# Optimization experiments

Measured on AMD Instinct MI355X. Metric: run time of the kernel, lower is better.

## Reference

```python
import jax, jax.numpy as jnp
import numpy as np

B, IN, J, K = 1024, 512, 64, 8
CLAMP_MAX = 10.0

def setup_inputs() -> dict:
    key = jax.random.key(0)
    k1, k2 = jax.random.split(key)
    x = jax.random.normal(k1, (B, IN), dtype=jnp.float32)
    T = jax.random.normal(k2, (IN, J, K), dtype=jnp.float32)
    return {"x": x, "T": T}

def reference(x, T):
    # M: [B, J, K]
    M = jnp.einsum('bi,ijk->bjk', x, T)
    # pairwise diff over batch: [B, B, J, K] (matches torch broadcast M1-M2)
    diff = M[None, :, :, :] - M[:, None, :, :]
    sq = jnp.sum(diff * diff, axis=3)          # [B, B, J]
    # safe sqrt (grad 0 at 0, matching torch.norm subgradient on diagonal)
    sq_safe = jnp.where(sq > 0, sq, 1.0)
    norm = jnp.where(sq > 0, jnp.sqrt(sq_safe), 0.0)
    c = jnp.exp(-jnp.minimum(norm, CLAMP_MAX))  # clamp(max=10) then exp(-.)
    feats = jnp.sum(c, axis=1)                  # [B, J]
    return jnp.concatenate([x, feats], axis=1)  # [B, IN + J]
```

## Files before the change

kernel.cpp:

```cpp
#include <hip/hip_runtime.h>

constexpr int NB  = 1024;
constexpr int NIN = 512;
constexpr int NJ  = 64;
constexpr int NK  = 8;
constexpr int NC  = NJ * NK;
constexpr int OUTC = NIN + NJ;
constexpr float EXPN10 = 4.5399929762484854e-05f;
constexpr float FEAT_BASE = 1024.0f * EXPN10;

typedef __bf16 bf16x8 __attribute__((ext_vector_type(8)));
typedef float floatx16 __attribute__((ext_vector_type(16)));

__device__ __forceinline__ unsigned f2bf(float f) {
  unsigned u = __float_as_uint(f);
  u += 0x7FFFu + ((u >> 16) & 1u);
  return u >> 16;
}

__global__ __launch_bounds__(256) void gemm_fused(const float* __restrict__ x,
                                                  const float* __restrict__ T,
                                                  float* __restrict__ Mp,
                                                  uint4* __restrict__ Mb,
                                                  float* __restrict__ na,
                                                  float* __restrict__ out) {
  __shared__ __align__(16) ushort smem_u[2 * 64 * 136];
  ushort* Xs = smem_u;
  ushort* Ts = smem_u + 64 * 136;
  float*  Cs = (float*)smem_u;

  const int tid = threadIdx.x;
  const int b0 = blockIdx.x * 64;
  const int c0 = blockIdx.y * 64;

  const int lane = tid & 63;
  const int w    = tid >> 6;
  const int l31  = lane & 31;
  const int half = lane >> 5;
  const int arow = (w & 1) * 32 + l31;
  const int bcol = (w >> 1) * 32 + l31;

  const int pr   = tid >> 4;
  const int coff = (tid & 15) * 4;

  const int bidf = blockIdx.y * 16 + blockIdx.x;
#pragma unroll
  for (int it = 0; it < 5; ++it) {
    const int li = it * 256 + tid;
    if (li < 1152) {
      const int gi = bidf * 1152 + li;
      const int b = gi / (OUTC / 4);
      const int r = gi - b * (OUTC / 4);
      float4 v;
      if (r < NIN / 4) v = ((const float4*)x)[b * (NIN / 4) + r];
      else v = float4{FEAT_BASE, FEAT_BASE, FEAT_BASE, FEAT_BASE};
      ((float4*)out)[gi] = v;
    }
  }

  floatx16 acc = {};

  for (int z = 0; z < 4; ++z) {
    float4 av[8];
#pragma unroll
    for (int t = 0; t < 4; ++t) {
      const int u = t * 256 + tid;
      const int row = u >> 4, seg = u & 15;
      const size_t base = (size_t)(b0 + row) * NIN + z * 128 + seg * 8;
      av[2 * t]     = *(const float4*)&x[base];
      av[2 * t + 1] = *(const float4*)&x[base + 4];
    }
    float4 bv[8];
#pragma unroll
    for (int it = 0; it < 4; ++it) {
      const int k0 = it * 32 + pr * 2;
      const size_t base = (size_t)(z * 128 + k0) * NC + c0 + coff;
      bv[2 * it]     = *(const float4*)&T[base];
      bv[2 * it + 1] = *(const float4*)&T[base + NC];
    }

#pragma unroll
    for (int t = 0; t < 4; ++t) {
      const int u = t * 256 + tid;
      const int row = u >> 4, seg = u & 15;
      uint4 p;
      p.x = f2bf(av[2 * t].x) | (f2bf(av[2 * t].y) << 16);
      p.y = f2bf(av[2 * t].z) | (f2bf(av[2 * t].w) << 16);
      p.z = f2bf(av[2 * t + 1].x) | (f2bf(av[2 * t + 1].y) << 16);
      p.w = f2bf(av[2 * t + 1].z) | (f2bf(av[2 * t + 1].w) << 16);
      *(uint4*)&Xs[row * 136 + seg * 8] = p;
    }
    unsigned* Tw = (unsigned*)Ts;
#pragma unroll
    for (int it = 0; it < 4; ++it) {
      const float* lo = &bv[2 * it].x;
      const float* hi = &bv[2 * it + 1].x;
#pragma unroll
      for (int q = 0; q < 4; ++q) {
        const unsigned val = f2bf(lo[q]) | (f2bf(hi[q]) << 16);
        Tw[(coff + q) * 68 + it * 16 + pr] = val;
      }
    }

    __syncthreads();

#pragma unroll
    for (int s = 0; s < 8; ++s) {
      const bf16x8 af = *(const bf16x8*)&Xs[arow * 136 + s * 16 + half * 8];
      const bf16x8 bf = *(const bf16x8*)&Ts[bcol * 136 + s * 16 + half * 8];
      acc = __builtin_amdgcn_mfma_f32_32x32x16_bf16(af, bf, acc, 0, 0, 0);
    }
    __syncthreads();
  }

#pragma unroll
  for (int reg = 0; reg < 16; ++reg) {
    const int row = (reg & 3) + 8 * (reg >> 2) + 4 * half;
    Cs[((w & 1) * 32 + row) * 68 + (w >> 1) * 32 + l31] = acc[reg];
  }
  __syncthreads();

#pragma unroll
  for (int pass = 0; pass < 2; ++pass) {
    const int jl = (tid >> 6) + pass * 4;
    const int b  = tid & 63;
    const float4 m0 = *(const float4*)&Cs[b * 68 + jl * 8];
    const float4 m1 = *(const float4*)&Cs[b * 68 + jl * 8 + 4];
    const int j_g = blockIdx.y * 8 + jl;
    const int idx = j_g * NB + b0 + b;
    ((float4*)Mp)[idx * 2]     = m0;
    ((float4*)Mp)[idx * 2 + 1] = m1;
    float s = m0.x * m0.x;
    s = fmaf(m0.y, m0.y, s); s = fmaf(m0.z, m0.z, s); s = fmaf(m0.w, m0.w, s);
    s = fmaf(m1.x, m1.x, s); s = fmaf(m1.y, m1.y, s); s = fmaf(m1.z, m1.z, s);
    s = fmaf(m1.w, m1.w, s);
    na[idx] = s;
    uint4 pk;
    pk.x = f2bf(m0.x) | (f2bf(m0.y) << 16);
    pk.y = f2bf(m0.z) | (f2bf(m0.w) << 16);
    pk.z = f2bf(m1.x) | (f2bf(m1.y) << 16);
    pk.w = f2bf(m1.z) | (f2bf(m1.w) << 16);
    Mb[idx] = pk;
  }
}

__global__ __launch_bounds__(256) void pairwise_kernel(const uint4* __restrict__ Mb,
                                                       const float* __restrict__ na,
                                                       const float* __restrict__ Mp,
                                                       float* __restrict__ out) {
  const int j    = blockIdx.x;
  const int ag   = blockIdx.y;
  const int bh   = blockIdx.z;
  const int tid  = threadIdx.x;
  const int lane = tid & 63;
  const int w    = tid >> 6;
  const int col  = lane & 31;
  const int h    = lane >> 5;
  const int jb   = j * NB;

  __shared__ uint4 Mb_s[513];
  __shared__ float nb_s[512];
  __shared__ float na_s[128];

  const int bbeg = bh * 512;
  Mb_s[tid]       = Mb[jb + bbeg + tid];
  Mb_s[tid + 256] = Mb[jb + bbeg + tid + 256];
  nb_s[tid]       = na[jb + bbeg + tid];
  nb_s[tid + 256] = na[jb + bbeg + tid + 256];
  if (tid == 0) Mb_s[512] = uint4{0u, 0u, 0u, 0u};

  const int a0 = ag * 128 + w * 32;
  if (lane < 32) na_s[w * 32 + lane] = na[jb + a0 + lane];

  uint4 araw = uint4{0u, 0u, 0u, 0u};
  if (lane < 32) araw = Mb[jb + a0 + lane];
  const bf16x8 af = __builtin_bit_cast(bf16x8, araw);

  __syncthreads();

  float c995[16];
#pragma unroll
  for (int reg = 0; reg < 16; ++reg) {
    const int row = (reg & 3) + 8 * (reg >> 2) + 4 * h;
    c995[reg] = 0.995f * na_s[w * 32 + row];
  }

  const floatx16 zero = {};

#pragma unroll 2
  for (int bt = 0; bt < 16; ++bt) {
    const int bidx = bt * 32 + col;
    const uint4 braw = Mb_s[lane < 32 ? bidx : 512];
    const bf16x8 bf = __builtin_bit_cast(bf16x8, braw);
    const floatx16 P = __builtin_amdgcn_mfma_f32_32x32x16_bf16(af, bf, zero, 0, 0, 0);
    const float nb_l = nb_s[bidx];
    const float rhs = 100.0f - 0.995f * nb_l;

    float t = fmaf(-2.0f, P[0], c995[0]);
#pragma unroll
    for (int reg = 1; reg < 16; ++reg)
      t = fminf(t, fmaf(-2.0f, P[reg], c995[reg]));

    if (__any(t < rhs)) {
#pragma unroll
      for (int reg = 0; reg < 16; ++reg) {
        if (fmaf(-2.0f, P[reg], c995[reg]) < rhs) {
          const int row = (reg & 3) + 8 * (reg >> 2) + 4 * h;
          const int a = a0 + row;
          const int b = bbeg + bt * 32 + col;
          float corr;
          if (a == b) {
            corr = 1.0f - EXPN10;
          } else {
            const float4 av0 = ((const float4*)Mp)[(jb + a) * 2];
            const float4 av1 = ((const float4*)Mp)[(jb + a) * 2 + 1];
            const float4 bv0 = ((const float4*)Mp)[(jb + b) * 2];
            const float4 bv1 = ((const float4*)Mp)[(jb + b) * 2 + 1];
            float d = av0.x - bv0.x; float sq = d * d;
            d = av0.y - bv0.y; sq = fmaf(d, d, sq);
            d = av0.z - bv0.z; sq = fmaf(d, d, sq);
            d = av0.w - bv0.w; sq = fmaf(d, d, sq);
            d = av1.x - bv1.x; sq = fmaf(d, d, sq);
            d = av1.y - bv1.y; sq = fmaf(d, d, sq);
            d = av1.z - bv1.z; sq = fmaf(d, d, sq);
            d = av1.w - bv1.w; sq = fmaf(d, d, sq);
            const float nrm = sqrtf(sq);
            corr = (nrm < 10.0f) ? (__expf(-nrm) - EXPN10) : 0.0f;
          }
          if (corr != 0.0f) atomicAdd(&out[a * OUTC + NIN + j], corr);
        }
      }
    }
  }
}

extern "C" void kernel_launch(void* const* d_in, const int* in_sizes, int n_in,
                              void* d_out, int out_size, void* d_ws, size_t ws_size,
                              hipStream_t stream) {
  const float* x = (const float*)d_in[0];
  const float* T = (const float*)d_in[1];
  float* out = (float*)d_out;

  float* Mp  = (float*)d_ws;
  float* na  = Mp + (size_t)NJ * NB * NK;
  uint4* Mb  = (uint4*)(na + (size_t)NJ * NB);

  gemm_fused<<<dim3(16, 8), 256, 0, stream>>>(x, T, Mp, Mb, na, out);
  pairwise_kernel<<<dim3(NJ, 8, 2), 256, 0, stream>>>(Mb, na, Mp, out);
}
```

Baseline: 74.69 us.

## Split GEMM columns in half and use split-K across warps

The GEMM tile shrinks from 64 to 32 output columns, so the grid doubles from 128 to 256 blocks. Within each block the four warps now split the K dimension in two halves instead of splitting columns, and the two partial 64x32 results are summed through shared memory before the epilogue. The aim is better CU occupancy on a GPU with many CUs, since the old grid left most of them idle. In exchange, each block reads the same x rows, so x traffic doubles, and the block uses more LDS plus an extra reduction step.

```diff
diff --git a/kernel.cpp b/kernel.cpp
--- a/kernel.cpp
+++ b/kernel.cpp
@@ -24,31 +24,32 @@
                                                   uint4* __restrict__ Mb,
                                                   float* __restrict__ na,
                                                   float* __restrict__ out) {
-  __shared__ __align__(16) ushort smem_u[2 * 64 * 136];
+  __shared__ __align__(16) ushort smem_u[2 * 64 * 136 + 2 * 32 * 136];
   ushort* Xs = smem_u;
-  ushort* Ts = smem_u + 64 * 136;
+  ushort* Ts = smem_u + 2 * 64 * 136;
   float*  Cs = (float*)smem_u;
 
   const int tid = threadIdx.x;
   const int b0 = blockIdx.x * 64;
-  const int c0 = blockIdx.y * 64;
+  const int c0 = blockIdx.y * 32;
 
   const int lane = tid & 63;
   const int w    = tid >> 6;
   const int l31  = lane & 31;
   const int half = lane >> 5;
-  const int arow = (w & 1) * 32 + l31;
-  const int bcol = (w >> 1) * 32 + l31;
-
-  const int pr   = tid >> 4;
-  const int coff = (tid & 15) * 4;
+  const int wr   = w & 1;
+  const int kh   = w >> 1;
+  const int arow = wr * 32 + l31;
+
+  const int bk = tid >> 3;
+  const int bc = (tid & 7) * 4;
 
   const int bidf = blockIdx.y * 16 + blockIdx.x;
 #pragma unroll
-  for (int it = 0; it < 5; ++it) {
+  for (int it = 0; it < 3; ++it) {
     const int li = it * 256 + tid;
-    if (li < 1152) {
-      const int gi = bidf * 1152 + li;
+    if (li < 576) {
+      const int gi = bidf * 576 + li;
       const int b = gi / (OUTC / 4);
       const int r = gi - b * (OUTC / 4);
       float4 v;
@@ -60,45 +61,54 @@
 
   floatx16 acc = {};
 
-  for (int z = 0; z < 4; ++z) {
-    float4 av[8];
-#pragma unroll
-    for (int t = 0; t < 4; ++t) {
-      const int u = t * 256 + tid;
-      const int row = u >> 4, seg = u & 15;
-      const size_t base = (size_t)(b0 + row) * NIN + z * 128 + seg * 8;
-      av[2 * t]     = *(const float4*)&x[base];
-      av[2 * t + 1] = *(const float4*)&x[base + 4];
+  for (int z = 0; z < 2; ++z) {
+    float4 av[16];
+#pragma unroll
+    for (int kk = 0; kk < 2; ++kk) {
+#pragma unroll
+      for (int t = 0; t < 4; ++t) {
+        const int u = t * 256 + tid;
+        const int row = u >> 4, seg = u & 15;
+        const size_t base = (size_t)(b0 + row) * NIN + (kk * 2 + z) * 128 + seg * 8;
+        av[kk * 8 + 2 * t]     = *(const float4*)&x[base];
+        av[kk * 8 + 2 * t + 1] = *(const float4*)&x[base + 4];
+      }
     }
     float4 bv[8];
 #pragma unroll
-    for (int it = 0; it < 4; ++it) {
-      const int k0 = it * 32 + pr * 2;
-      const size_t base = (size_t)(z * 128 + k0) * NC + c0 + coff;
-      bv[2 * it]     = *(const float4*)&T[base];
-      bv[2 * it + 1] = *(const float4*)&T[base + NC];
-    }
-
-#pragma unroll
-    for (int t = 0; t < 4; ++t) {
-      const int u = t * 256 + tid;
-      const int row = u >> 4, seg = u & 15;
-      uint4 p;
-      p.x = f2bf(av[2 * t].x) | (f2bf(av[2 * t].y) << 16);
-      p.y = f2bf(av[2 * t].z) | (f2bf(av[2 * t].w) << 16);
-      p.z = f2bf(av[2 * t + 1].x) | (f2bf(av[2 * t + 1].y) << 16);
-      p.w = f2bf(av[2 * t + 1].z) | (f2bf(av[2 * t + 1].w) << 16);
-      *(uint4*)&Xs[row * 136 + seg * 8] = p;
-    }
-    unsigned* Tw = (unsigned*)Ts;
-#pragma unroll
-    for (int it = 0; it < 4; ++it) {
-      const float* lo = &bv[2 * it].x;
-      const float* hi = &bv[2 * it + 1].x;
-#pragma unroll
-      for (int q = 0; q < 4; ++q) {
-        const unsigned val = f2bf(lo[q]) | (f2bf(hi[q]) << 16);
-        Tw[(coff + q) * 68 + it * 16 + pr] = val;
+    for (int kk = 0; kk < 2; ++kk) {
+#pragma unroll
+      for (int it = 0; it < 2; ++it) {
+        const int k0 = it * 64 + bk * 2;
+        const size_t base = (size_t)((kk * 2 + z) * 128 + k0) * NC + c0 + bc;
+        bv[kk * 4 + 2 * it]     = *(const float4*)&T[base];
+        bv[kk * 4 + 2 * it + 1] = *(const float4*)&T[base + NC];
+      }
+    }
+
+#pragma unroll
+    for (int kk = 0; kk < 2; ++kk) {
+#pragma unroll
+      for (int t = 0; t < 4; ++t) {
+        const int u = t * 256 + tid;
+        const int row = u >> 4, seg = u & 15;
+        uint4 p;
+        p.x = f2bf(av[kk * 8 + 2 * t].x) | (f2bf(av[kk * 8 + 2 * t].y) << 16);
+        p.y = f2bf(av[kk * 8 + 2 * t].z) | (f2bf(av[kk * 8 + 2 * t].w) << 16);
+        p.z = f2bf(av[kk * 8 + 2 * t + 1].x) | (f2bf(av[kk * 8 + 2 * t + 1].y) << 16);
+        p.w = f2bf(av[kk * 8 + 2 * t + 1].z) | (f2bf(av[kk * 8 + 2 * t + 1].w) << 16);
+        *(uint4*)&Xs[kk * 64 * 136 + row * 136 + seg * 8] = p;
+      }
+      unsigned* Tw = (unsigned*)(Ts + kk * 32 * 136);
+#pragma unroll
+      for (int it = 0; it < 2; ++it) {
+        const float* lo = &bv[kk * 4 + 2 * it].x;
+        const float* hi = &bv[kk * 4 + 2 * it + 1].x;
+#pragma unroll
+        for (int q = 0; q < 4; ++q) {
+          const unsigned val = f2bf(lo[q]) | (f2bf(hi[q]) << 16);
+          Tw[(bc + q) * 68 + it * 32 + bk] = val;
+        }
       }
     }
 
@@ -106,8 +116,8 @@
 
 #pragma unroll
     for (int s = 0; s < 8; ++s) {
-      const bf16x8 af = *(const bf16x8*)&Xs[arow * 136 + s * 16 + half * 8];
-      const bf16x8 bf = *(const bf16x8*)&Ts[bcol * 136 + s * 16 + half * 8];
+      const bf16x8 af = *(const bf16x8*)&Xs[kh * 64 * 136 + arow * 136 + s * 16 + half * 8];
+      const bf16x8 bf = *(const bf16x8*)&Ts[kh * 32 * 136 + l31 * 136 + s * 16 + half * 8];
       acc = __builtin_amdgcn_mfma_f32_32x32x16_bf16(af, bf, acc, 0, 0, 0);
     }
     __syncthreads();
@@ -116,17 +126,20 @@
 #pragma unroll
   for (int reg = 0; reg < 16; ++reg) {
     const int row = (reg & 3) + 8 * (reg >> 2) + 4 * half;
-    Cs[((w & 1) * 32 + row) * 68 + (w >> 1) * 32 + l31] = acc[reg];
+    Cs[kh * 64 * 36 + (wr * 32 + row) * 36 + l31] = acc[reg];
   }
   __syncthreads();
 
-#pragma unroll
-  for (int pass = 0; pass < 2; ++pass) {
-    const int jl = (tid >> 6) + pass * 4;
+  {
+    const int jl = tid >> 6;
     const int b  = tid & 63;
-    const float4 m0 = *(const float4*)&Cs[b * 68 + jl * 8];
-    const float4 m1 = *(const float4*)&Cs[b * 68 + jl * 8 + 4];
-    const int j_g = blockIdx.y * 8 + jl;
+    const float4 p0 = *(const float4*)&Cs[b * 36 + jl * 8];
+    const float4 p1 = *(const float4*)&Cs[b * 36 + jl * 8 + 4];
+    const float4 q0 = *(const float4*)&Cs[64 * 36 + b * 36 + jl * 8];
+    const float4 q1 = *(const float4*)&Cs[64 * 36 + b * 36 + jl * 8 + 4];
+    const float4 m0 = float4{p0.x + q0.x, p0.y + q0.y, p0.z + q0.z, p0.w + q0.w};
+    const float4 m1 = float4{p1.x + q1.x, p1.y + q1.y, p1.z + q1.z, p1.w + q1.w};
+    const int j_g = blockIdx.y * 4 + jl;
     const int idx = j_g * NB + b0 + b;
     ((float4*)Mp)[idx * 2]     = m0;
     ((float4*)Mp)[idx * 2 + 1] = m1;
@@ -245,6 +258,6 @@
   float* na  = Mp + (size_t)NJ * NB * NK;
   uint4* Mb  = (uint4*)(na + (size_t)NJ * NB);
 
-  gemm_fused<<<dim3(16, 8), 256, 0, stream>>>(x, T, Mp, Mb, na, out);
+  gemm_fused<<<dim3(16, 16), 256, 0, stream>>>(x, T, Mp, Mb, na, out);
   pairwise_kernel<<<dim3(NJ, 8, 2), 256, 0, stream>>>(Mb, na, Mp, out);
 }
```

After: 72.15 us. 1.04x faster.

## Split GEMM K dimension across waves with smaller 32x32 tiles and more blocks

Applied to the files above, without the earlier changes.

The projection GEMM moves from 64x64 tiles with a sequential four-step K loop to 32x32 output tiles, which gives four times as many blocks. Each of the four waves handles one 128-wide K quarter, and the partial results are summed through shared memory. All x and T loads are issued up front in a single stage, removing the per-iteration barriers and giving 512 blocks instead of 128 to fill the GPU. The cost is more total global reads of x and T, more registers per thread, and an extra shared-memory reduction.

```diff
diff --git a/kernel.cpp b/kernel.cpp
--- a/kernel.cpp
+++ b/kernel.cpp
@@ -18,115 +18,122 @@
   return u >> 16;
 }
 
-__global__ __launch_bounds__(256) void gemm_fused(const float* __restrict__ x,
-                                                  const float* __restrict__ T,
-                                                  float* __restrict__ Mp,
-                                                  uint4* __restrict__ Mb,
-                                                  float* __restrict__ na,
-                                                  float* __restrict__ out) {
-  __shared__ __align__(16) ushort smem_u[2 * 64 * 136];
+__global__ __launch_bounds__(256, 2) void gemm_fused(const float* __restrict__ x,
+                                                     const float* __restrict__ T,
+                                                     float* __restrict__ Mp,
+                                                     uint4* __restrict__ Mb,
+                                                     float* __restrict__ na,
+                                                     float* __restrict__ out) {
+  __shared__ __align__(16) ushort smem_u[2 * 4 * 32 * 136];
   ushort* Xs = smem_u;
-  ushort* Ts = smem_u + 64 * 136;
+  ushort* Ts = smem_u + 4 * 32 * 136;
   float*  Cs = (float*)smem_u;
 
   const int tid = threadIdx.x;
-  const int b0 = blockIdx.x * 64;
-  const int c0 = blockIdx.y * 64;
+  const int b0 = blockIdx.x * 32;
+  const int c0 = blockIdx.y * 32;
 
   const int lane = tid & 63;
   const int w    = tid >> 6;
   const int l31  = lane & 31;
   const int half = lane >> 5;
-  const int arow = (w & 1) * 32 + l31;
-  const int bcol = (w >> 1) * 32 + l31;
-
-  const int pr   = tid >> 4;
-  const int coff = (tid & 15) * 4;
-
-  const int bidf = blockIdx.y * 16 + blockIdx.x;
-#pragma unroll
-  for (int it = 0; it < 5; ++it) {
-    const int li = it * 256 + tid;
-    if (li < 1152) {
-      const int gi = bidf * 1152 + li;
-      const int b = gi / (OUTC / 4);
-      const int r = gi - b * (OUTC / 4);
-      float4 v;
-      if (r < NIN / 4) v = ((const float4*)x)[b * (NIN / 4) + r];
-      else v = float4{FEAT_BASE, FEAT_BASE, FEAT_BASE, FEAT_BASE};
-      ((float4*)out)[gi] = v;
-    }
-  }
+
+  const int bidf = blockIdx.y * 32 + blockIdx.x;
+  {
+    const int gi0 = bidf * 288;
+#pragma unroll
+    for (int it = 0; it < 2; ++it) {
+      const int li = it * 256 + tid;
+      if (li < 288) {
+        const int gi = gi0 + li;
+        const int b = gi / (OUTC / 4);
+        const int r = gi - b * (OUTC / 4);
+        float4 v;
+        if (r < NIN / 4) v = ((const float4*)x)[b * (NIN / 4) + r];
+        else v = float4{FEAT_BASE, FEAT_BASE, FEAT_BASE, FEAT_BASE};
+        ((float4*)out)[gi] = v;
+      }
+    }
+  }
+
+  float4 av[16];
+#pragma unroll
+  for (int t = 0; t < 8; ++t) {
+    const int u = t * 256 + tid;
+    const int kq  = u >> 9;
+    const int row = (u >> 4) & 31;
+    const int seg = u & 15;
+    const size_t base = (size_t)(b0 + row) * NIN + kq * 128 + seg * 8;
+    av[2 * t]     = *(const float4*)&x[base];
+    av[2 * t + 1] = *(const float4*)&x[base + 4];
+  }
+  float4 bv[16];
+#pragma unroll
+  for (int it = 0; it < 8; ++it) {
+    const int k0 = it * 64 + (tid >> 3) * 2;
+    const size_t base = (size_t)k0 * NC + c0 + (tid & 7) * 4;
+    bv[2 * it]     = *(const float4*)&T[base];
+    bv[2 * it + 1] = *(const float4*)&T[base + NC];
+  }
+
+#pragma unroll
+  for (int t = 0; t < 8; ++t) {
+    const int u = t * 256 + tid;
+    const int kq  = u >> 9;
+    const int row = (u >> 4) & 31;
+    const int seg = u & 15;
+    uint4 p;
+    p.x = f2bf(av[2 * t].x) | (f2bf(av[2 * t].y) << 16);
+    p.y = f2bf(av[2 * t].z) | (f2bf(av[2 * t].w) << 16);
+    p.z = f2bf(av[2 * t + 1].x) | (f2bf(av[2 * t + 1].y) << 16);
+    p.w = f2bf(av[2 * t + 1].z) | (f2bf(av[2 * t + 1].w) << 16);
+    *(uint4*)&Xs[kq * 32 * 136 + row * 136 + seg * 8] = p;
+  }
+#pragma unroll
+  for (int it = 0; it < 8; ++it) {
+    const int kq = it >> 1;
+    const int kd = (it & 1) * 32 + (tid >> 3);
+    unsigned* Tw = (unsigned*)(Ts + kq * 32 * 136);
+    const float* lo = &bv[2 * it].x;
+    const float* hi = &bv[2 * it + 1].x;
+#pragma unroll
+    for (int q = 0; q < 4; ++q) {
+      const unsigned val = f2bf(lo[q]) | (f2bf(hi[q]) << 16);
+      Tw[((tid & 7) * 4 + q) * 68 + kd] = val;
+    }
+  }
+
+  __syncthreads();
 
   floatx16 acc = {};
-
-  for (int z = 0; z < 4; ++z) {
-    float4 av[8];
-#pragma unroll
-    for (int t = 0; t < 4; ++t) {
-      const int u = t * 256 + tid;
-      const int row = u >> 4, seg = u & 15;
-      const size_t base = (size_t)(b0 + row) * NIN + z * 128 + seg * 8;
-      av[2 * t]     = *(const float4*)&x[base];
-      av[2 * t + 1] = *(const float4*)&x[base + 4];
-    }
-    float4 bv[8];
-#pragma unroll
-    for (int it = 0; it < 4; ++it) {
-      const int k0 = it * 32 + pr * 2;
-      const size_t base = (size_t)(z * 128 + k0) * NC + c0 + coff;
-      bv[2 * it]     = *(const float4*)&T[base];
-      bv[2 * it + 1] = *(const float4*)&T[base + NC];
-    }
-
-#pragma unroll
-    for (int t = 0; t < 4; ++t) {
-      const int u = t * 256 + tid;
-      const int row = u >> 4, seg = u & 15;
-      uint4 p;
-      p.x = f2bf(av[2 * t].x) | (f2bf(av[2 * t].y) << 16);
-      p.y = f2bf(av[2 * t].z) | (f2bf(av[2 * t].w) << 16);
-      p.z = f2bf(av[2 * t + 1].x) | (f2bf(av[2 * t + 1].y) << 16);
-      p.w = f2bf(av[2 * t + 1].z) | (f2bf(av[2 * t + 1].w) << 16);
-      *(uint4*)&Xs[row * 136 + seg * 8] = p;
-    }
-    unsigned* Tw = (unsigned*)Ts;
-#pragma unroll
-    for (int it = 0; it < 4; ++it) {
-      const float* lo = &bv[2 * it].x;
-      const float* hi = &bv[2 * it + 1].x;
-#pragma unroll
-      for (int q = 0; q < 4; ++q) {
-        const unsigned val = f2bf(lo[q]) | (f2bf(hi[q]) << 16);
-        Tw[(coff + q) * 68 + it * 16 + pr] = val;
-      }
-    }
-
-    __syncthreads();
-
-#pragma unroll
-    for (int s = 0; s < 8; ++s) {
-      const bf16x8 af = *(const bf16x8*)&Xs[arow * 136 + s * 16 + half * 8];
-      const bf16x8 bf = *(const bf16x8*)&Ts[bcol * 136 + s * 16 + half * 8];
-      acc = __builtin_amdgcn_mfma_f32_32x32x16_bf16(af, bf, acc, 0, 0, 0);
-    }
-    __syncthreads();
-  }
+#pragma unroll
+  for (int s = 0; s < 8; ++s) {
+    const bf16x8 af = *(const bf16x8*)&Xs[w * 32 * 136 + l31 * 136 + s * 16 + half * 8];
+    const bf16x8 bf = *(const bf16x8*)&Ts[w * 32 * 136 + l31 * 136 + s * 16 + half * 8];
+    acc = __builtin_amdgcn_mfma_f32_32x32x16_bf16(af, bf, acc, 0, 0, 0);
+  }
+  __syncthreads();
 
 #pragma unroll
   for (int reg = 0; reg < 16; ++reg) {
     const int row = (reg & 3) + 8 * (reg >> 2) + 4 * half;
-    Cs[((w & 1) * 32 + row) * 68 + (w >> 1) * 32 + l31] = acc[reg];
-  }
-  __syncthreads();
-
-#pragma unroll
-  for (int pass = 0; pass < 2; ++pass) {
-    const int jl = (tid >> 6) + pass * 4;
-    const int b  = tid & 63;
-    const float4 m0 = *(const float4*)&Cs[b * 68 + jl * 8];
-    const float4 m1 = *(const float4*)&Cs[b * 68 + jl * 8 + 4];
-    const int j_g = blockIdx.y * 8 + jl;
+    Cs[w * 32 * 36 + row * 36 + l31] = acc[reg];
+  }
+  __syncthreads();
+
+  if (tid < 128) {
+    const int b  = tid & 31;
+    const int jl = tid >> 5;
+    float4 m0 = float4{0.f, 0.f, 0.f, 0.f};
+    float4 m1 = float4{0.f, 0.f, 0.f, 0.f};
+#pragma unroll
+    for (int kq = 0; kq < 4; ++kq) {
+      const float4 p0 = *(const float4*)&Cs[kq * 32 * 36 + b * 36 + jl * 8];
+      const float4 p1 = *(const float4*)&Cs[kq * 32 * 36 + b * 36 + jl * 8 + 4];
+      m0.x += p0.x; m0.y += p0.y; m0.z += p0.z; m0.w += p0.w;
+      m1.x += p1.x; m1.y += p1.y; m1.z += p1.z; m1.w += p1.w;
+    }
+    const int j_g = blockIdx.y * 4 + jl;
     const int idx = j_g * NB + b0 + b;
     ((float4*)Mp)[idx * 2]     = m0;
     ((float4*)Mp)[idx * 2 + 1] = m1;
@@ -245,6 +252,6 @@
   float* na  = Mp + (size_t)NJ * NB * NK;
   uint4* Mb  = (uint4*)(na + (size_t)NJ * NB);
 
-  gemm_fused<<<dim3(16, 8), 256, 0, stream>>>(x, T, Mp, Mb, na, out);
+  gemm_fused<<<dim3(32, 16), 256, 0, stream>>>(x, T, Mp, Mb, na, out);
   pairwise_kernel<<<dim3(NJ, 8, 2), 256, 0, stream>>>(Mb, na, Mp, out);
 }
```

After: 72.58 us. -2.8%, faster.
